# Performance work log

Measured on AMD Instinct MI355X. Metric: run time of the kernel, lower is better.

Reference implementation:

```python
import jax, jax.numpy as jnp
import numpy as np

N = 50000      # nodes
E = 400000     # directed edges
F_IN = 128     # input features
H0, C0 = 4, 64     # layer0: 4 heads x 64, concat -> 256
H1, C1 = 1, 256    # layer1: 1 head x 256, mean/concat -> 256
NCLS = 10
SLOPE = 0.2    # PyG GATConv leaky_relu negative_slope


def setup_inputs() -> dict:
    key = jax.random.key(0)
    ks = jax.random.split(key, 20)
    g = lambda k, shape, fan_in: jax.random.normal(k, shape, jnp.float32) * (1.0 / np.sqrt(fan_in))
    x = jax.random.normal(ks[0], (N, F_IN), jnp.float32)
    edge_index = jax.random.randint(ks[1], (2, E), 0, N)
    return {
        "x": x,
        "edge_index": edge_index,
        # GATConv layer 0: 128 -> 4 heads x 64, concat
        "W0": g(ks[2], (F_IN, H0 * C0), F_IN),
        "a_src0": g(ks[3], (H0, C0), C0),
        "a_dst0": g(ks[4], (H0, C0), C0),
        "b0": jnp.zeros((H0 * C0,), jnp.float32),
        # GATConv layer 1: 256 -> 1 head x 256, averaged
        "W1": g(ks[5], (H0 * C0, H1 * C1), H0 * C0),
        "a_src1": g(ks[6], (H1, C1), C1),
        "a_dst1": g(ks[7], (H1, C1), C1),
        "b1": jnp.zeros((C1,), jnp.float32),
        # MLP head 256 -> 512 -> 1024 -> NCLS
        "lw1": g(ks[8], (256, 512), 256), "lb1": jnp.zeros((512,), jnp.float32),
        "lw2": g(ks[9], (512, 1024), 512), "lb2": jnp.zeros((1024,), jnp.float32),
        "lw3": g(ks[10], (1024, NCLS), 1024), "lb3": jnp.zeros((NCLS,), jnp.float32),
    }


def _gat_conv(x, src, dst, valid, W, a_src, a_dst, b, heads, ch, concat):
    """PyG GATConv (eval mode, dropout=0): gather -> edge attention ->
    softmax over incoming edges per target -> scatter-sum aggregate."""
    n = x.shape[0]
    h = (x @ W).reshape(n, heads, ch)                      # [N,H,C]
    alpha_src = jnp.sum(h * a_src[None], axis=-1)          # [N,H]
    alpha_dst = jnp.sum(h * a_dst[None], axis=-1)          # [N,H]
    e = jax.nn.leaky_relu(alpha_src[src] + alpha_dst[dst], SLOPE)  # [Etot,H]
    e = jnp.where(valid[:, None], e, -1e9)                 # removed self-loops
    emax = jax.lax.stop_gradient(jax.ops.segment_max(e, dst, num_segments=n))
    w = jnp.exp(e - emax[dst]) * valid[:, None].astype(e.dtype)
    denom = jax.ops.segment_sum(w, dst, num_segments=n)    # [N,H] (>0: self-loops)
    w = w / denom[dst]
    out = jax.ops.segment_sum(h[src] * w[..., None], dst, num_segments=n)  # [N,H,C]
    out = out.reshape(n, heads * ch) if concat else out.mean(axis=1)
    return out + b


def reference(x, edge_index, W0, a_src0, a_dst0, b0, W1, a_src1, a_dst1, b1,
              lw1, lb1, lw2, lb2, lw3, lb3):
    n = x.shape[0]
    s0, d0 = edge_index[0], edge_index[1]
    loop = jnp.arange(n, dtype=s0.dtype)
    src = jnp.concatenate([s0, loop])
    dst = jnp.concatenate([d0, loop])
    valid = jnp.concatenate([s0 != d0, jnp.ones((n,), bool)])  # remove+add self-loops
    h = jax.nn.relu(_gat_conv(x, src, dst, valid, W0, a_src0, a_dst0, b0, H0, C0, True))
    h = jax.nn.relu(_gat_conv(h, src, dst, valid, W1, a_src1, a_dst1, b1, H1, C1, False))
    h = jax.nn.relu(h @ lw1 + lb1)
    h = jax.nn.relu(h @ lw2 + lb2)
    h = jax.nn.relu(h @ lw3 + lb3)
    return jax.nn.softmax(h, axis=1)
```

## Files before the change

### kernel.cpp

```cpp
#include <hip/hip_runtime.h>
#include <cstdint>
#include <cstddef>

#define F_IN   128
#define SLOPE  0.2f

typedef unsigned short u16;
typedef __attribute__((ext_vector_type(8))) short     bf16x8;
typedef __attribute__((ext_vector_type(8))) unsigned short u16x8;
typedef __attribute__((ext_vector_type(4))) unsigned short u16x4;
typedef __attribute__((ext_vector_type(4))) float     f32x4;

__device__ __forceinline__ u16 f2bf(float f) {
    unsigned u = __float_as_uint(f);
    unsigned r = u + 0x7FFFu + ((u >> 16) & 1u);
    return (u16)(r >> 16);
}
__device__ __forceinline__ float bf2f(u16 h) {
    return __uint_as_float(((unsigned)h) << 16);
}

__device__ __forceinline__ float lrelu(float v) { return v >= 0.f ? v : SLOPE * v; }

__global__ void alphas0_k(const float* __restrict__ h0, const float* __restrict__ a_src,
                          const float* __restrict__ a_dst, float* __restrict__ asrc,
                          float* __restrict__ adst, int N) {
    int gid = blockIdx.x * blockDim.x + threadIdx.x;
    int n = gid >> 6, lane = gid & 63;
    if (n >= N) return;
    #pragma unroll
    for (int h = 0; h < 4; ++h) {
        float v  = h0[(size_t)n * 256 + h * 64 + lane];
        float s1 = v * a_src[h * 64 + lane];
        float s2 = v * a_dst[h * 64 + lane];
        #pragma unroll
        for (int off = 32; off; off >>= 1) {
            s1 += __shfl_down(s1, off);
            s2 += __shfl_down(s2, off);
        }
        if (lane == 0) { asrc[n * 4 + h] = s1; adst[n * 4 + h] = s2; }
    }
}

__global__ void alphas1_k(const float* __restrict__ h1, const float* __restrict__ a_src,
                          const float* __restrict__ a_dst, float* __restrict__ asrc,
                          float* __restrict__ adst, int N) {
    int gid = blockIdx.x * blockDim.x + threadIdx.x;
    int n = gid >> 6, lane = gid & 63;
    if (n >= N) return;
    float s1 = 0.f, s2 = 0.f;
    #pragma unroll
    for (int k = 0; k < 4; ++k) {
        float v = h1[(size_t)n * 256 + k * 64 + lane];
        s1 += v * a_src[k * 64 + lane];
        s2 += v * a_dst[k * 64 + lane];
    }
    #pragma unroll
    for (int off = 32; off; off >>= 1) {
        s1 += __shfl_down(s1, off);
        s2 += __shfl_down(s2, off);
    }
    if (lane == 0) { asrc[n] = s1; adst[n] = s2; }
}

__global__ void deg_init(int* __restrict__ deg, int N) {
    int i = blockIdx.x * blockDim.x + threadIdx.x;
    if (i < N) deg[i] = 1;
}

__global__ void count_deg(const int* __restrict__ ei, int* __restrict__ deg, int E) {
    int e = blockIdx.x * blockDim.x + threadIdx.x;
    if (e >= E) return;
    int s = ei[e], d = ei[E + e];
    if (s != d) atomicAdd(&deg[d], 1);
}

__global__ void scan1(const int* __restrict__ deg, int* __restrict__ part,
                      int* __restrict__ bsum, int N) {
    __shared__ int sm[256];
    int i = blockIdx.x * 256 + threadIdx.x;
    int v = (i < N) ? deg[i] : 0;
    sm[threadIdx.x] = v; __syncthreads();
    for (int off = 1; off < 256; off <<= 1) {
        int tv = (threadIdx.x >= off) ? sm[threadIdx.x - off] : 0;
        __syncthreads();
        sm[threadIdx.x] += tv;
        __syncthreads();
    }
    if (i < N) part[i] = sm[threadIdx.x] - v;
    if (threadIdx.x == 255) bsum[blockIdx.x] = sm[255];
}

__global__ void scan2(int* __restrict__ bsum, int nb) {
    __shared__ int sm[256];
    __shared__ int carry;
    if (threadIdx.x == 0) carry = 0;
    __syncthreads();
    for (int base = 0; base < nb; base += 256) {
        int i = base + threadIdx.x;
        int v = (i < nb) ? bsum[i] : 0;
        sm[threadIdx.x] = v; __syncthreads();
        for (int off = 1; off < 256; off <<= 1) {
            int tv = (threadIdx.x >= off) ? sm[threadIdx.x - off] : 0;
            __syncthreads();
            sm[threadIdx.x] += tv;
            __syncthreads();
        }
        if (i < nb) bsum[i] = sm[threadIdx.x] - v + carry;
        __syncthreads();
        if (threadIdx.x == 0) carry += sm[255];
        __syncthreads();
    }
}

__global__ void scan3(const int* __restrict__ deg, const int* __restrict__ part,
                      const int* __restrict__ bsum, int* __restrict__ rowp,
                      int* __restrict__ cursor, int N) {
    int i = blockIdx.x * blockDim.x + threadIdx.x;
    if (i >= N) return;
    int r = part[i] + bsum[i >> 8];
    rowp[i] = r;
    cursor[i] = r;
    if (i == N - 1) rowp[N] = r + deg[i];
}

__global__ void scatter_k(const int* __restrict__ ei, int* __restrict__ cursor,
                          int* __restrict__ csr, int E, int N) {
    int e = blockIdx.x * blockDim.x + threadIdx.x;
    if (e >= E + N) return;
    int s, d;
    if (e < E) { s = ei[e]; d = ei[E + e]; if (s == d) return; }
    else       { s = d = e - E; }
    int pos = atomicAdd(&cursor[d], 1);
    csr[pos] = s;
}

__global__ void gat_gather0(const int* __restrict__ csr, const int* __restrict__ rowp,
                            const float* __restrict__ h0, const float* __restrict__ asrc,
                            const float* __restrict__ adst, const float* __restrict__ b,
                            float* __restrict__ outx, int N) {
    int gid = blockIdx.x * blockDim.x + threadIdx.x;
    int n = gid >> 6, lane = gid & 63;
    if (n >= N) return;
    int beg = rowp[n], end = rowp[n + 1];
    float4 ad = *(const float4*)(adst + (size_t)n * 4);
    float m0 = -1e30f, m1 = -1e30f, m2 = -1e30f, m3 = -1e30f;
    for (int i = beg + lane; i < end; i += 64) {
        int s = csr[i];
        float4 as = *(const float4*)(asrc + (size_t)s * 4);
        m0 = fmaxf(m0, lrelu(as.x + ad.x));
        m1 = fmaxf(m1, lrelu(as.y + ad.y));
        m2 = fmaxf(m2, lrelu(as.z + ad.z));
        m3 = fmaxf(m3, lrelu(as.w + ad.w));
    }
    #pragma unroll
    for (int off = 32; off; off >>= 1) {
        m0 = fmaxf(m0, __shfl_xor(m0, off));
        m1 = fmaxf(m1, __shfl_xor(m1, off));
        m2 = fmaxf(m2, __shfl_xor(m2, off));
        m3 = fmaxf(m3, __shfl_xor(m3, off));
    }
    float acc0 = 0.f, acc1 = 0.f, acc2 = 0.f, acc3 = 0.f;
    float den0 = 0.f, den1 = 0.f, den2 = 0.f, den3 = 0.f;
    for (int i = beg; i < end; ++i) {
        int s = csr[i];
        float4 as = *(const float4*)(asrc + (size_t)s * 4);
        float w0 = __expf(lrelu(as.x + ad.x) - m0);
        float w1 = __expf(lrelu(as.y + ad.y) - m1);
        float w2 = __expf(lrelu(as.z + ad.z) - m2);
        float w3 = __expf(lrelu(as.w + ad.w) - m3);
        den0 += w0; den1 += w1; den2 += w2; den3 += w3;
        const float* hs = h0 + (size_t)s * 256;
        acc0 += w0 * hs[lane];
        acc1 += w1 * hs[64 + lane];
        acc2 += w2 * hs[128 + lane];
        acc3 += w3 * hs[192 + lane];
    }
    float* po = outx + (size_t)n * 256;
    float v;
    v = acc0 / den0 + b[lane];       po[lane]       = v > 0.f ? v : 0.f;
    v = acc1 / den1 + b[64 + lane];  po[64 + lane]  = v > 0.f ? v : 0.f;
    v = acc2 / den2 + b[128 + lane]; po[128 + lane] = v > 0.f ? v : 0.f;
    v = acc3 / den3 + b[192 + lane]; po[192 + lane] = v > 0.f ? v : 0.f;
}

__global__ void gat_gather1(const int* __restrict__ csr, const int* __restrict__ rowp,
                            const float* __restrict__ h1, const float* __restrict__ asrc,
                            const float* __restrict__ adst, const float* __restrict__ b,
                            float* __restrict__ outx, int N) {
    int gid = blockIdx.x * blockDim.x + threadIdx.x;
    int n = gid >> 6, lane = gid & 63;
    if (n >= N) return;
    int beg = rowp[n], end = rowp[n + 1];
    float adn = adst[n];
    float mx = -1e30f;
    for (int i = beg + lane; i < end; i += 64) {
        int s = csr[i];
        mx = fmaxf(mx, lrelu(asrc[s] + adn));
    }
    #pragma unroll
    for (int off = 32; off; off >>= 1) mx = fmaxf(mx, __shfl_xor(mx, off));
    float acc0 = 0.f, acc1 = 0.f, acc2 = 0.f, acc3 = 0.f, den = 0.f;
    for (int i = beg; i < end; ++i) {
        int s = csr[i];
        float w = __expf(lrelu(asrc[s] + adn) - mx);
        den += w;
        const float* hs = h1 + (size_t)s * 256;
        acc0 += w * hs[lane];
        acc1 += w * hs[64 + lane];
        acc2 += w * hs[128 + lane];
        acc3 += w * hs[192 + lane];
    }
    float inv = 1.f / den;
    float* po = outx + (size_t)n * 256;
    float v;
    v = acc0 * inv + b[lane];       po[lane]       = v > 0.f ? v : 0.f;
    v = acc1 * inv + b[64 + lane];  po[64 + lane]  = v > 0.f ? v : 0.f;
    v = acc2 * inv + b[128 + lane]; po[128 + lane] = v > 0.f ? v : 0.f;
    v = acc3 * inv + b[192 + lane]; po[192 + lane] = v > 0.f ? v : 0.f;
}

__global__ void pack_w(const float* __restrict__ W, u16* __restrict__ out,
                       int K, int Nsrc, int NT) {
    int gid  = blockIdx.x * blockDim.x + threadIdx.x;
    int lane = gid & 63, frag = gid >> 6;
    int KT = K >> 5;
    if (frag >= KT * NT) return;
    int nt = frag % NT, kt = frag / NT;
    int n  = nt * 16 + (lane & 15);
    int k0 = kt * 32 + ((lane >> 4) << 3);
    u16x8 v8;
    #pragma unroll
    for (int i = 0; i < 8; ++i) {
        float v = (n < Nsrc) ? W[(size_t)(k0 + i) * Nsrc + n] : 0.f;
        v8[i] = f2bf(v);
    }
    *(u16x8*)(out + (size_t)(frag * 64 + lane) * 8) = v8;
}

__global__ void pack_w_hl(const float* __restrict__ W, u16* __restrict__ ohi,
                          u16* __restrict__ olo, int K, int Nsrc, int NT) {
    int gid  = blockIdx.x * blockDim.x + threadIdx.x;
    int lane = gid & 63, frag = gid >> 6;
    int KT = K >> 5;
    if (frag >= KT * NT) return;
    int nt = frag % NT, kt = frag / NT;
    int n  = nt * 16 + (lane & 15);
    int k0 = kt * 32 + ((lane >> 4) << 3);
    u16x8 h8, l8;
    #pragma unroll
    for (int i = 0; i < 8; ++i) {
        float v = (n < Nsrc) ? W[(size_t)(k0 + i) * Nsrc + n] : 0.f;
        u16 hi = f2bf(v);
        h8[i] = hi;
        l8[i] = f2bf(v - bf2f(hi));
    }
    *(u16x8*)(ohi + (size_t)(frag * 64 + lane) * 8) = h8;
    *(u16x8*)(olo + (size_t)(frag * 64 + lane) * 8) = l8;
}

__device__ __forceinline__ bf16x8 lds_afrag(const u16* buf, int Kdim, int row0, int kt, int lane) {
    int row = row0 + (lane & 15);
    int k   = kt * 32 + ((lane >> 4) << 3);
    int idx = (row * Kdim + k) ^ ((row & 7) << 3);
    return *(const bf16x8*)(buf + idx);
}

__global__ __launch_bounds__(512) void gemm_mfma(
    const float* __restrict__ A, const u16* __restrict__ bhi, const u16* __restrict__ blo,
    float* __restrict__ C, int M, int K) {
    __shared__ __align__(16) u16 Ahi[64 * 256];
    __shared__ __align__(16) u16 Alo[64 * 256];
    int t = threadIdx.x, lane = t & 63, w = t >> 6;
    int row0 = blockIdx.x * 64;
    int K4 = K >> 2;

    for (int idx = t; idx < 64 * K4; idx += 512) {
        int row = idx / K4, kq = (idx % K4) << 2;
        int gr = row0 + row;
        float4 v = make_float4(0.f, 0.f, 0.f, 0.f);
        if (gr < M) v = *(const float4*)(A + (size_t)gr * K + kq);
        u16x4 h4, l4;
        float vv[4] = {v.x, v.y, v.z, v.w};
        #pragma unroll
        for (int i = 0; i < 4; ++i) {
            u16 hi = f2bf(vv[i]);
            h4[i] = hi;
            l4[i] = f2bf(vv[i] - bf2f(hi));
        }
        int sidx = (row * K + kq) ^ ((row & 7) << 3);
        *(u16x4*)(Ahi + sidx) = h4;
        *(u16x4*)(Alo + sidx) = l4;
    }
    __syncthreads();

    int KT = K >> 5;
    f32x4 acc[4][2] = {};
    for (int kt = 0; kt < KT; ++kt) {
        bf16x8 ah[4], al[4];
        #pragma unroll
        for (int mt = 0; mt < 4; ++mt) {
            ah[mt] = lds_afrag(Ahi, K, mt * 16, kt, lane);
            al[mt] = lds_afrag(Alo, K, mt * 16, kt, lane);
        }
        #pragma unroll
        for (int nt = 0; nt < 2; ++nt) {
            int ntg = w * 2 + nt;
            size_t fo = ((size_t)(kt * 16 + ntg) * 64 + lane) * 8;
            bf16x8 bh = *(const bf16x8*)(bhi + fo);
            bf16x8 bl = *(const bf16x8*)(blo + fo);
            #pragma unroll
            for (int mt = 0; mt < 4; ++mt) {
                acc[mt][nt] = __builtin_amdgcn_mfma_f32_16x16x32_bf16(al[mt], bh, acc[mt][nt], 0, 0, 0);
                acc[mt][nt] = __builtin_amdgcn_mfma_f32_16x16x32_bf16(ah[mt], bl, acc[mt][nt], 0, 0, 0);
                acc[mt][nt] = __builtin_amdgcn_mfma_f32_16x16x32_bf16(ah[mt], bh, acc[mt][nt], 0, 0, 0);
            }
        }
    }

    #pragma unroll
    for (int mt = 0; mt < 4; ++mt)
        #pragma unroll
        for (int nt = 0; nt < 2; ++nt) {
            int col = w * 32 + nt * 16 + (lane & 15);
            #pragma unroll
            for (int j = 0; j < 4; ++j) {
                int gr = row0 + mt * 16 + ((lane >> 4) << 2) + j;
                if (gr < M) C[(size_t)gr * 256 + col] = acc[mt][nt][j];
            }
        }
}

#define NB 32

__global__ __launch_bounds__(512) void mlp_mfma(
    const float* __restrict__ m0,
    const u16* __restrict__ w1p, const float* __restrict__ lb1,
    const u16* __restrict__ w2p, const float* __restrict__ lb2,
    const u16* __restrict__ w3p, const float* __restrict__ lb3,
    float* __restrict__ out, int N) {
    __shared__ __align__(16) u16 ldsA0[32 * 256];
    __shared__ __align__(16) u16 ldsA1[32 * 512];
    __shared__ __align__(16) u16 ldsA2[32 * 1024];
    __shared__ float slog[32 * 16];

    int t = threadIdx.x, lane = t & 63, w = t >> 6;
    int nb = blockIdx.x * NB;

    slog[t] = 0.f;

    bf16x8 b1A[4], b1B[4];
    #pragma unroll
    for (int nt = 0; nt < 4; ++nt)
        b1A[nt] = *(const bf16x8*)(w1p + ((size_t)(w * 4 + nt) * 64 + lane) * 8);

    #pragma unroll
    for (int u = 0; u < 2; ++u) {
        int unit = t + u * 512;
        int row = unit >> 5, kb = (unit & 31) << 3;
        int gn = nb + row;
        u16x8 v8;
        if (gn < N) {
            const float4* p = (const float4*)(m0 + (size_t)gn * 256 + kb);
            float4 x0 = p[0], x1 = p[1];
            v8[0] = f2bf(x0.x); v8[1] = f2bf(x0.y); v8[2] = f2bf(x0.z); v8[3] = f2bf(x0.w);
            v8[4] = f2bf(x1.x); v8[5] = f2bf(x1.y); v8[6] = f2bf(x1.z); v8[7] = f2bf(x1.w);
        } else {
            v8 = (u16x8)0;
        }
        int idx = (row * 256 + kb) ^ ((row & 7) << 3);
        *(u16x8*)(ldsA0 + idx) = v8;
    }
    __syncthreads();

    f32x4 acc1[2][4] = {};
    for (int kt = 0; kt < 8; kt += 2) {
        #pragma unroll
        for (int nt = 0; nt < 4; ++nt)
            b1B[nt] = *(const bf16x8*)(w1p + ((size_t)((kt + 1) * 32 + w * 4 + nt) * 64 + lane) * 8);
        {
            bf16x8 a0 = lds_afrag(ldsA0, 256, 0,  kt, lane);
            bf16x8 a1 = lds_afrag(ldsA0, 256, 16, kt, lane);
            #pragma unroll
            for (int nt = 0; nt < 4; ++nt) {
                acc1[0][nt] = __builtin_amdgcn_mfma_f32_16x16x32_bf16(a0, b1A[nt], acc1[0][nt], 0, 0, 0);
                acc1[1][nt] = __builtin_amdgcn_mfma_f32_16x16x32_bf16(a1, b1A[nt], acc1[1][nt], 0, 0, 0);
            }
        }
        if (kt + 2 < 8) {
            #pragma unroll
            for (int nt = 0; nt < 4; ++nt)
                b1A[nt] = *(const bf16x8*)(w1p + ((size_t)((kt + 2) * 32 + w * 4 + nt) * 64 + lane) * 8);
        }
        {
            bf16x8 a0 = lds_afrag(ldsA0, 256, 0,  kt + 1, lane);
            bf16x8 a1 = lds_afrag(ldsA0, 256, 16, kt + 1, lane);
            #pragma unroll
            for (int nt = 0; nt < 4; ++nt) {
                acc1[0][nt] = __builtin_amdgcn_mfma_f32_16x16x32_bf16(a0, b1B[nt], acc1[0][nt], 0, 0, 0);
                acc1[1][nt] = __builtin_amdgcn_mfma_f32_16x16x32_bf16(a1, b1B[nt], acc1[1][nt], 0, 0, 0);
            }
        }
    }

    bf16x8 b2A[8], b2B[8];
    #pragma unroll
    for (int nt = 0; nt < 8; ++nt)
        b2A[nt] = *(const bf16x8*)(w2p + ((size_t)(w * 8 + nt) * 64 + lane) * 8);

    #pragma unroll
    for (int mt = 0; mt < 2; ++mt)
        #pragma unroll
        for (int nt = 0; nt < 4; ++nt) {
            int col = w * 64 + nt * 16 + (lane & 15);
            float bv = lb1[col];
            #pragma unroll
            for (int j = 0; j < 4; ++j) {
                int row = mt * 16 + ((lane >> 4) << 2) + j;
                float v = acc1[mt][nt][j] + bv;
                v = v > 0.f ? v : 0.f;
                ldsA1[(row * 512 + col) ^ ((row & 7) << 3)] = f2bf(v);
            }
        }
    __syncthreads();

    f32x4 acc2[2][8] = {};
    for (int kt = 0; kt < 16; kt += 2) {
        #pragma unroll
        for (int nt = 0; nt < 8; ++nt)
            b2B[nt] = *(const bf16x8*)(w2p + ((size_t)((kt + 1) * 64 + w * 8 + nt) * 64 + lane) * 8);
        {
            bf16x8 a0 = lds_afrag(ldsA1, 512, 0,  kt, lane);
            bf16x8 a1 = lds_afrag(ldsA1, 512, 16, kt, lane);
            #pragma unroll
            for (int nt = 0; nt < 8; ++nt) {
                acc2[0][nt] = __builtin_amdgcn_mfma_f32_16x16x32_bf16(a0, b2A[nt], acc2[0][nt], 0, 0, 0);
                acc2[1][nt] = __builtin_amdgcn_mfma_f32_16x16x32_bf16(a1, b2A[nt], acc2[1][nt], 0, 0, 0);
            }
        }
        if (kt + 2 < 16) {
            #pragma unroll
            for (int nt = 0; nt < 8; ++nt)
                b2A[nt] = *(const bf16x8*)(w2p + ((size_t)((kt + 2) * 64 + w * 8 + nt) * 64 + lane) * 8);
        }
        {
            bf16x8 a0 = lds_afrag(ldsA1, 512, 0,  kt + 1, lane);
            bf16x8 a1 = lds_afrag(ldsA1, 512, 16, kt + 1, lane);
            #pragma unroll
            for (int nt = 0; nt < 8; ++nt) {
                acc2[0][nt] = __builtin_amdgcn_mfma_f32_16x16x32_bf16(a0, b2B[nt], acc2[0][nt], 0, 0, 0);
                acc2[1][nt] = __builtin_amdgcn_mfma_f32_16x16x32_bf16(a1, b2B[nt], acc2[1][nt], 0, 0, 0);
            }
        }
    }

    bf16x8 b3[4];
    #pragma unroll
    for (int kk = 0; kk < 4; ++kk)
        b3[kk] = *(const bf16x8*)(w3p + ((size_t)(w * 4 + kk) * 64 + lane) * 8);

    #pragma unroll
    for (int mt = 0; mt < 2; ++mt)
        #pragma unroll
        for (int nt = 0; nt < 8; ++nt) {
            int col = w * 128 + nt * 16 + (lane & 15);
            float bv = lb2[col];
            #pragma unroll
            for (int j = 0; j < 4; ++j) {
                int row = mt * 16 + ((lane >> 4) << 2) + j;
                float v = acc2[mt][nt][j] + bv;
                v = v > 0.f ? v : 0.f;
                ldsA2[(row * 1024 + col) ^ ((row & 7) << 3)] = f2bf(v);
            }
        }
    __syncthreads();

    {
        f32x4 acc[2] = {};
        #pragma unroll
        for (int kk = 0; kk < 4; ++kk) {
            int kt = w * 4 + kk;
            bf16x8 a0 = lds_afrag(ldsA2, 1024, 0,  kt, lane);
            bf16x8 a1 = lds_afrag(ldsA2, 1024, 16, kt, lane);
            acc[0] = __builtin_amdgcn_mfma_f32_16x16x32_bf16(a0, b3[kk], acc[0], 0, 0, 0);
            acc[1] = __builtin_amdgcn_mfma_f32_16x16x32_bf16(a1, b3[kk], acc[1], 0, 0, 0);
        }
        int col = lane & 15;
        #pragma unroll
        for (int mt = 0; mt < 2; ++mt)
            #pragma unroll
            for (int j = 0; j < 4; ++j) {
                int row = mt * 16 + ((lane >> 4) << 2) + j;
                atomicAdd(&slog[row * 16 + col], acc[mt][j]);
            }
    }
    __syncthreads();

    if (t < 32) {
        int gn = nb + t;
        if (gn < N) {
            float lg[10], m = -1e30f;
            #pragma unroll
            for (int k = 0; k < 10; ++k) {
                float v = slog[t * 16 + k] + lb3[k];
                v = v > 0.f ? v : 0.f;
                lg[k] = v;
                if (v > m) m = v;
            }
            float ssum = 0.f;
            #pragma unroll
            for (int k = 0; k < 10; ++k) { lg[k] = __expf(lg[k] - m); ssum += lg[k]; }
            float inv = 1.f / ssum;
            #pragma unroll
            for (int k = 0; k < 10; ++k) out[(size_t)gn * 10 + k] = lg[k] * inv;
        }
    }
}

extern "C" void kernel_launch(void* const* d_in, const int* in_sizes, int n_in,
                              void* d_out, int out_size, void* d_ws, size_t ws_size,
                              hipStream_t stream) {
    const float* x       = (const float*)d_in[0];
    const int*   ei      = (const int*)  d_in[1];
    const float* W0      = (const float*)d_in[2];
    const float* a_src0  = (const float*)d_in[3];
    const float* a_dst0  = (const float*)d_in[4];
    const float* b0      = (const float*)d_in[5];
    const float* W1      = (const float*)d_in[6];
    const float* a_src1  = (const float*)d_in[7];
    const float* a_dst1  = (const float*)d_in[8];
    const float* b1      = (const float*)d_in[9];
    const float* lw1     = (const float*)d_in[10];
    const float* lb1     = (const float*)d_in[11];
    const float* lw2     = (const float*)d_in[12];
    const float* lb2     = (const float*)d_in[13];
    const float* lw3     = (const float*)d_in[14];
    const float* lb3     = (const float*)d_in[15];
    float*       out     = (float*)d_out;

    const int N  = in_sizes[0] / F_IN;
    const int E  = in_sizes[1] / 2;
    const int ET = E + N;

    float* ws   = (float*)d_ws;
    size_t szH  = (size_t)N * 256;
    float* bufH = ws;
    float* bufG = ws + szH;
    float* asrc = ws + 2 * szH;
    float* adst = asrc + (size_t)N * 4;
    u16*   w1p  = (u16*)(adst + (size_t)N * 4);
    u16*   w2p  = w1p + 256 * 512;
    u16*   w3p  = w2p + 512 * 1024;
    u16*   w0h  = w3p + 1024 * 16;
    u16*   w0l  = w0h + 128 * 256;
    u16*   w1h  = w0l + 128 * 256;
    u16*   w1l  = w1h + 256 * 256;
    int*   deg  = (int*)(w1l + 256 * 256);
    int*   rowp   = deg + N;
    int*   cursor = rowp + N + 1;
    int*   part   = cursor + N;
    int*   bsum   = part + N;
    int*   csr    = bsum + 256;

    const int TB  = 256;
    const int nb1 = (N + 255) / 256;
    const int gemm_grid = (N + 63) / 64;

    pack_w<<<(8  * 32 * 64 + TB - 1) / TB, TB, 0, stream>>>(lw1, w1p, 256,  512,  32);
    pack_w<<<(16 * 64 * 64 + TB - 1) / TB, TB, 0, stream>>>(lw2, w2p, 512,  1024, 64);
    pack_w<<<(32 * 1  * 64 + TB - 1) / TB, TB, 0, stream>>>(lw3, w3p, 1024, 10,   1);
    pack_w_hl<<<(4 * 16 * 64 + TB - 1) / TB, TB, 0, stream>>>(W0, w0h, w0l, 128, 256, 16);
    pack_w_hl<<<(8 * 16 * 64 + TB - 1) / TB, TB, 0, stream>>>(W1, w1h, w1l, 256, 256, 16);

    deg_init<<<nb1, TB, 0, stream>>>(deg, N);
    count_deg<<<(E + TB - 1) / TB, TB, 0, stream>>>(ei, deg, E);
    scan1<<<nb1, TB, 0, stream>>>(deg, part, bsum, N);
    scan2<<<1, TB, 0, stream>>>(bsum, nb1);
    scan3<<<nb1, TB, 0, stream>>>(deg, part, bsum, rowp, cursor, N);
    scatter_k<<<(ET + TB - 1) / TB, TB, 0, stream>>>(ei, cursor, csr, E, N);

    gemm_mfma<<<gemm_grid, 512, 0, stream>>>(x, w0h, w0l, bufH, N, 128);
    alphas0_k<<<(N * 64 + TB - 1) / TB, TB, 0, stream>>>(bufH, a_src0, a_dst0, asrc, adst, N);
    gat_gather0<<<((size_t)N * 64 + TB - 1) / TB, TB, 0, stream>>>(csr, rowp, bufH, asrc, adst, b0, bufG, N);

    gemm_mfma<<<gemm_grid, 512, 0, stream>>>(bufG, w1h, w1l, bufH, N, 256);
    alphas1_k<<<(N * 64 + TB - 1) / TB, TB, 0, stream>>>(bufH, a_src1, a_dst1, asrc, adst, N);
    gat_gather1<<<((size_t)N * 64 + TB - 1) / TB, TB, 0, stream>>>(csr, rowp, bufH, asrc, adst, b1, bufG, N);

    mlp_mfma<<<(N + NB - 1) / NB, 512, 0, stream>>>(bufG, w1p, lb1, w2p, lb2, w3p, lb3, out, N);
}
```

Baseline: 453.6 us.

## Store GAT projected features and layer-1 output in bf16 to halve gather traffic

The GEMM outputs (projected node features h) are now written as bf16 instead of fp32, and the alpha and gather kernels read them as bf16 and widen to float. The second gather also writes its output directly in bf16, so the MLP kernel loads bf16 without converting. This roughly halves the bytes moved by the random neighbour gathers and the intermediate writes and reads. The cost is extra rounding error in the attention logits and aggregated features, and the 16-bit per-lane gather loads are narrower and may coalesce less well.

```diff
diff --git a/kernel.cpp b/kernel.cpp
--- a/kernel.cpp
+++ b/kernel.cpp
@@ -22,7 +22,7 @@
 
 __device__ __forceinline__ float lrelu(float v) { return v >= 0.f ? v : SLOPE * v; }
 
-__global__ void alphas0_k(const float* __restrict__ h0, const float* __restrict__ a_src,
+__global__ void alphas0_k(const u16* __restrict__ h0, const float* __restrict__ a_src,
                           const float* __restrict__ a_dst, float* __restrict__ asrc,
                           float* __restrict__ adst, int N) {
     int gid = blockIdx.x * blockDim.x + threadIdx.x;
@@ -30,7 +30,7 @@
     if (n >= N) return;
     #pragma unroll
     for (int h = 0; h < 4; ++h) {
-        float v  = h0[(size_t)n * 256 + h * 64 + lane];
+        float v  = bf2f(h0[(size_t)n * 256 + h * 64 + lane]);
         float s1 = v * a_src[h * 64 + lane];
         float s2 = v * a_dst[h * 64 + lane];
         #pragma unroll
@@ -42,7 +42,7 @@
     }
 }
 
-__global__ void alphas1_k(const float* __restrict__ h1, const float* __restrict__ a_src,
+__global__ void alphas1_k(const u16* __restrict__ h1, const float* __restrict__ a_src,
                           const float* __restrict__ a_dst, float* __restrict__ asrc,
                           float* __restrict__ adst, int N) {
     int gid = blockIdx.x * blockDim.x + threadIdx.x;
@@ -51,7 +51,7 @@
     float s1 = 0.f, s2 = 0.f;
     #pragma unroll
     for (int k = 0; k < 4; ++k) {
-        float v = h1[(size_t)n * 256 + k * 64 + lane];
+        float v = bf2f(h1[(size_t)n * 256 + k * 64 + lane]);
         s1 += v * a_src[k * 64 + lane];
         s2 += v * a_dst[k * 64 + lane];
     }
@@ -136,7 +136,7 @@
 }
 
 __global__ void gat_gather0(const int* __restrict__ csr, const int* __restrict__ rowp,
-                            const float* __restrict__ h0, const float* __restrict__ asrc,
+                            const u16* __restrict__ h0, const float* __restrict__ asrc,
                             const float* __restrict__ adst, const float* __restrict__ b,
                             float* __restrict__ outx, int N) {
     int gid = blockIdx.x * blockDim.x + threadIdx.x;
@@ -170,11 +170,11 @@
         float w2 = __expf(lrelu(as.z + ad.z) - m2);
         float w3 = __expf(lrelu(as.w + ad.w) - m3);
         den0 += w0; den1 += w1; den2 += w2; den3 += w3;
-        const float* hs = h0 + (size_t)s * 256;
-        acc0 += w0 * hs[lane];
-        acc1 += w1 * hs[64 + lane];
-        acc2 += w2 * hs[128 + lane];
-        acc3 += w3 * hs[192 + lane];
+        const u16* hs = h0 + (size_t)s * 256;
+        acc0 += w0 * bf2f(hs[lane]);
+        acc1 += w1 * bf2f(hs[64 + lane]);
+        acc2 += w2 * bf2f(hs[128 + lane]);
+        acc3 += w3 * bf2f(hs[192 + lane]);
     }
     float* po = outx + (size_t)n * 256;
     float v;
@@ -185,9 +185,9 @@
 }
 
 __global__ void gat_gather1(const int* __restrict__ csr, const int* __restrict__ rowp,
-                            const float* __restrict__ h1, const float* __restrict__ asrc,
+                            const u16* __restrict__ h1, const float* __restrict__ asrc,
                             const float* __restrict__ adst, const float* __restrict__ b,
-                            float* __restrict__ outx, int N) {
+                            u16* __restrict__ outx, int N) {
     int gid = blockIdx.x * blockDim.x + threadIdx.x;
     int n = gid >> 6, lane = gid & 63;
     if (n >= N) return;
@@ -205,19 +205,19 @@
         int s = csr[i];
         float w = __expf(lrelu(asrc[s] + adn) - mx);
         den += w;
-        const float* hs = h1 + (size_t)s * 256;
-        acc0 += w * hs[lane];
-        acc1 += w * hs[64 + lane];
-        acc2 += w * hs[128 + lane];
-        acc3 += w * hs[192 + lane];
+        const u16* hs = h1 + (size_t)s * 256;
+        acc0 += w * bf2f(hs[lane]);
+        acc1 += w * bf2f(hs[64 + lane]);
+        acc2 += w * bf2f(hs[128 + lane]);
+        acc3 += w * bf2f(hs[192 + lane]);
     }
     float inv = 1.f / den;
-    float* po = outx + (size_t)n * 256;
+    u16* po = outx + (size_t)n * 256;
     float v;
-    v = acc0 * inv + b[lane];       po[lane]       = v > 0.f ? v : 0.f;
-    v = acc1 * inv + b[64 + lane];  po[64 + lane]  = v > 0.f ? v : 0.f;
-    v = acc2 * inv + b[128 + lane]; po[128 + lane] = v > 0.f ? v : 0.f;
-    v = acc3 * inv + b[192 + lane]; po[192 + lane] = v > 0.f ? v : 0.f;
+    v = acc0 * inv + b[lane];       po[lane]       = f2bf(v > 0.f ? v : 0.f);
+    v = acc1 * inv + b[64 + lane];  po[64 + lane]  = f2bf(v > 0.f ? v : 0.f);
+    v = acc2 * inv + b[128 + lane]; po[128 + lane] = f2bf(v > 0.f ? v : 0.f);
+    v = acc3 * inv + b[192 + lane]; po[192 + lane] = f2bf(v > 0.f ? v : 0.f);
 }
 
 __global__ void pack_w(const float* __restrict__ W, u16* __restrict__ out,
@@ -268,7 +268,7 @@
 
 __global__ __launch_bounds__(512) void gemm_mfma(
     const float* __restrict__ A, const u16* __restrict__ bhi, const u16* __restrict__ blo,
-    float* __restrict__ C, int M, int K) {
+    u16* __restrict__ C, int M, int K) {
     __shared__ __align__(16) u16 Ahi[64 * 256];
     __shared__ __align__(16) u16 Alo[64 * 256];
     int t = threadIdx.x, lane = t & 63, w = t >> 6;
@@ -326,7 +326,7 @@
             #pragma unroll
             for (int j = 0; j < 4; ++j) {
                 int gr = row0 + mt * 16 + ((lane >> 4) << 2) + j;
-                if (gr < M) C[(size_t)gr * 256 + col] = acc[mt][nt][j];
+                if (gr < M) C[(size_t)gr * 256 + col] = f2bf(acc[mt][nt][j]);
             }
         }
 }
@@ -334,7 +334,7 @@
 #define NB 32
 
 __global__ __launch_bounds__(512) void mlp_mfma(
-    const float* __restrict__ m0,
+    const u16* __restrict__ m0,
     const u16* __restrict__ w1p, const float* __restrict__ lb1,
     const u16* __restrict__ w2p, const float* __restrict__ lb2,
     const u16* __restrict__ w3p, const float* __restrict__ lb3,
@@ -360,14 +360,8 @@
         int row = unit >> 5, kb = (unit & 31) << 3;
         int gn = nb + row;
         u16x8 v8;
-        if (gn < N) {
-            const float4* p = (const float4*)(m0 + (size_t)gn * 256 + kb);
-            float4 x0 = p[0], x1 = p[1];
-            v8[0] = f2bf(x0.x); v8[1] = f2bf(x0.y); v8[2] = f2bf(x0.z); v8[3] = f2bf(x0.w);
-            v8[4] = f2bf(x1.x); v8[5] = f2bf(x1.y); v8[6] = f2bf(x1.z); v8[7] = f2bf(x1.w);
-        } else {
-            v8 = (u16x8)0;
-        }
+        if (gn < N) v8 = *(const u16x8*)(m0 + (size_t)gn * 256 + kb);
+        else        v8 = (u16x8)0;
         int idx = (row * 256 + kb) ^ ((row & 7) << 3);
         *(u16x8*)(ldsA0 + idx) = v8;
     }
@@ -542,11 +536,12 @@
     const int E  = in_sizes[1] / 2;
     const int ET = E + N;
 
-    float* ws   = (float*)d_ws;
-    size_t szH  = (size_t)N * 256;
-    float* bufH = ws;
-    float* bufG = ws + szH;
-    float* asrc = ws + 2 * szH;
+    char* base = (char*)d_ws;
+    size_t szHb = (size_t)N * 256 * sizeof(u16);
+    u16*   hbf  = (u16*)base;
+    float* bufG = (float*)(base + szHb);
+    u16*   m0b  = (u16*)(base + szHb + (size_t)N * 256 * sizeof(float));
+    float* asrc = (float*)(base + 2 * szHb + (size_t)N * 256 * sizeof(float));
     float* adst = asrc + (size_t)N * 4;
     u16*   w1p  = (u16*)(adst + (size_t)N * 4);
     u16*   w2p  = w1p + 256 * 512;
@@ -579,13 +574,13 @@
     scan3<<<nb1, TB, 0, stream>>>(deg, part, bsum, rowp, cursor, N);
     scatter_k<<<(ET + TB - 1) / TB, TB, 0, stream>>>(ei, cursor, csr, E, N);
 
-    gemm_mfma<<<gemm_grid, 512, 0, stream>>>(x, w0h, w0l, bufH, N, 128);
-    alphas0_k<<<(N * 64 + TB - 1) / TB, TB, 0, stream>>>(bufH, a_src0, a_dst0, asrc, adst, N);
-    gat_gather0<<<((size_t)N * 64 + TB - 1) / TB, TB, 0, stream>>>(csr, rowp, bufH, asrc, adst, b0, bufG, N);
-
-    gemm_mfma<<<gemm_grid, 512, 0, stream>>>(bufG, w1h, w1l, bufH, N, 256);
-    alphas1_k<<<(N * 64 + TB - 1) / TB, TB, 0, stream>>>(bufH, a_src1, a_dst1, asrc, adst, N);
-    gat_gather1<<<((size_t)N * 64 + TB - 1) / TB, TB, 0, stream>>>(csr, rowp, bufH, asrc, adst, b1, bufG, N);
-
-    mlp_mfma<<<(N + NB - 1) / NB, 512, 0, stream>>>(bufG, w1p, lb1, w2p, lb2, w3p, lb3, out, N);
-}
+    gemm_mfma<<<gemm_grid, 512, 0, stream>>>(x, w0h, w0l, hbf, N, 128);
+    alphas0_k<<<(N * 64 + TB - 1) / TB, TB, 0, stream>>>(hbf, a_src0, a_dst0, asrc, adst, N);
+    gat_gather0<<<((size_t)N * 64 + TB - 1) / TB, TB, 0, stream>>>(csr, rowp, hbf, asrc, adst, b0, bufG, N);
+
+    gemm_mfma<<<gemm_grid, 512, 0, stream>>>(bufG, w1h, w1l, hbf, N, 256);
+    alphas1_k<<<(N * 64 + TB - 1) / TB, TB, 0, stream>>>(hbf, a_src1, a_dst1, asrc, adst, N);
+    gat_gather1<<<((size_t)N * 64 + TB - 1) / TB, TB, 0, stream>>>(csr, rowp, hbf, asrc, adst, b1, m0b, N);
+
+    mlp_mfma<<<(N + NB - 1) / NB, 512, 0, stream>>>(m0b, w1p, lb1, w2p, lb2, w3p, lb3, out, N);
+}
```

Measured after the change: 429.0 us. -5.4%, faster.
